# Kernel tuning notes

Hardware: AMD Instinct MI355X
Metric: run time of the kernel (lower is better)

Reference implementation:

```python
import jax, jax.numpy as jnp
import numpy as np

N, C, H, W = 16, 512, 32, 32
NH = 8            # num_heads
HD = C // NH      # head dim c = 64
G = C // 4        # GroupNorm groups = 128
EPS = 1e-5


def conv1x1(X, Wt, b):
    # 1x1 Conv2d == per-pixel linear over channels
    return jnp.einsum('oc,nchw->nohw', Wt, X) + b[None, :, None, None]


def setup_inputs() -> dict:
    key = jax.random.key(0)
    ks = jax.random.split(key, 9)
    s = 0.02
    inp = {
        'X': jax.random.normal(ks[0], (N, C, H, W), jnp.float32),
        'Wq': jax.random.normal(ks[1], (C, C), jnp.float32) * s,
        'bq': jax.random.normal(ks[2], (C,), jnp.float32) * s,
        'Wk': jax.random.normal(ks[3], (C, C), jnp.float32) * s,
        'bk': jax.random.normal(ks[4], (C,), jnp.float32) * s,
        'Wv': jax.random.normal(ks[5], (C, C), jnp.float32) * s,
        'bv': jax.random.normal(ks[6], (C,), jnp.float32) * s,
        'Wo': jax.random.normal(ks[7], (C, C), jnp.float32) * s,
        'bo': jax.random.normal(ks[8], (C,), jnp.float32) * s,
        'gn_w': jnp.ones((C,), jnp.float32),
        'gn_b': jnp.zeros((C,), jnp.float32),
    }
    return inp


def reference(X, Wq, bq, Wk, bk, Wv, bv, Wo, bo, gn_w, gn_b):
    # NOTE: original torch code does  K, Q, V = (Q_conv(X), K_conv(X), V_conv(X))
    # i.e. K gets the Q_conv weights and Q gets the K_conv weights; mirror that.
    K = conv1x1(X, Wq, bq)
    Q = conv1x1(X, Wk, bk)
    V = conv1x1(X, Wv, bv)

    d = H * W
    Kh = K.reshape(N, NH, HD, d)  # [n,h,c,d]
    Qh = Q.reshape(N, NH, HD, d)
    Vh = V.reshape(N, NH, HD, d)

    # softmax-free channel attention: (Q^T K) then V (Q^T K)^T
    A = jnp.einsum('nhcd,nhcD->nhdD', Qh, Kh)   # [n,h,d,d]
    O = jnp.einsum('nhdD,nhcD->nhcd', A, Vh)    # [n,h,c,d]

    O = O.reshape(N, C, H, W)
    O = conv1x1(O, Wo, bo)

    # GroupNorm(G, C) with affine, eps=1e-5
    Og = O.reshape(N, G, C // G, H, W)
    mu = Og.mean(axis=(2, 3, 4), keepdims=True)
    var = Og.var(axis=(2, 3, 4), keepdims=True)
    On = ((Og - mu) * jax.lax.rsqrt(var + EPS)).reshape(N, C, H, W)
    On = On * gn_w[None, :, None, None] + gn_b[None, :, None, None]

    return On + X
```

## Files before the change

### kernel.cpp

```cpp
#include <hip/hip_runtime.h>
#include <hip/hip_bf16.h>

typedef __attribute__((ext_vector_type(8))) short s8v;
typedef __attribute__((ext_vector_type(4))) short s4v;
typedef __attribute__((ext_vector_type(4))) float f32x4;

#define MFMA_BF16 __builtin_amdgcn_mfma_f32_16x16x32_bf16

__device__ inline void gload_lds16(const __hip_bfloat16* g, __hip_bfloat16* l) {
  __builtin_amdgcn_global_load_lds(
      (const __attribute__((address_space(1))) void*)g,
      (__attribute__((address_space(3))) void*)l, 16, 0, 0);
}

__device__ inline short f2bs(float x) {
  __hip_bfloat16 b = __float2bfloat16(x);
  return *reinterpret_cast<short*>(&b);
}

__device__ inline void storeC(float* p, float v) { *p = v; }
__device__ inline void storeC(__hip_bfloat16* p, float v) { *p = __float2bfloat16(v); }

__global__ __launch_bounds__(256) void prep(const float* __restrict__ X,
                                            __hip_bfloat16* __restrict__ XT,
                                            __hip_bfloat16* __restrict__ Xc,
                                            const float* __restrict__ Wq,
                                            const float* __restrict__ Wv,
                                            const float* __restrict__ Wk,
                                            const float* __restrict__ Wo,
                                            const float* __restrict__ bq,
                                            const float* __restrict__ bv,
                                            __hip_bfloat16* __restrict__ WA,
                                            __hip_bfloat16* __restrict__ WkT,
                                            __hip_bfloat16* __restrict__ WOb,
                                            float* __restrict__ biasKV) {
  const int tid = threadIdx.x;
  if (blockIdx.z == 16) {
    const int blk = blockIdx.y * 16 + blockIdx.x;
#pragma unroll
    for (int t = 0; t < 8; ++t) {
      const int i = (blk * 8 + t) * 256 + tid;
      WA[i] = __float2bfloat16(Wq[i]);
      WA[262144 + i] = __float2bfloat16(Wv[i]);
      WOb[i] = __float2bfloat16(Wo[i]);
      WkT[i] = __float2bfloat16(Wk[(i & 511) * 512 + (i >> 9)]);
      if (i < 512) { biasKV[i] = bq[i]; biasKV[512 + i] = bv[i]; }
    }
    return;
  }
  __shared__ float tl[64][65];
  const int n = blockIdx.z;
  const int c0 = blockIdx.y * 64, p0 = blockIdx.x * 64;
  const int lr = tid >> 4, lc4 = (tid & 15) * 4;
  const float* Xp = X + ((long)n * 512 + c0) * 1024 + p0;
  __hip_bfloat16* Xcp = Xc + ((long)n * 512 + c0) * 1024 + p0;
#pragma unroll
  for (int i = 0; i < 4; ++i) {
    const int ch = i * 16 + lr;
    const float4 v = *(const float4*)&Xp[(long)ch * 1024 + lc4];
    tl[ch][lc4 + 0] = v.x; tl[ch][lc4 + 1] = v.y;
    tl[ch][lc4 + 2] = v.z; tl[ch][lc4 + 3] = v.w;
    s4v xo;
    xo[0] = f2bs(v.x); xo[1] = f2bs(v.y); xo[2] = f2bs(v.z); xo[3] = f2bs(v.w);
    *(s4v*)&Xcp[(long)ch * 1024 + lc4] = xo;
  }
  __syncthreads();
  __hip_bfloat16* XTp = XT + ((long)n * 1024 + p0) * 512 + c0;
#pragma unroll
  for (int i = 0; i < 4; ++i) {
    const int px = i * 16 + lr;
    s4v o;
#pragma unroll
    for (int e = 0; e < 4; ++e) o[e] = f2bs(tl[lc4 + e][px]);
    *(s4v*)&XTp[(long)px * 512 + lc4] = o;
  }
}

template <typename OutT, bool BROW>
__global__ __launch_bounds__(256) void gemm_nt(
    const __hip_bfloat16* __restrict__ A, long strideA,
    const __hip_bfloat16* __restrict__ B, long strideB,
    OutT* __restrict__ C, long strideC, int K, int ldc,
    const float* __restrict__ brow, long strideBrow) {
  A += blockIdx.z * strideA;
  B += blockIdx.z * strideB;
  C += blockIdx.z * strideC;
  const int m0 = blockIdx.y * 128;
  const int n0 = blockIdx.x * 128;
  const int tid = threadIdx.x;
  const int wid = tid >> 6, lane = tid & 63;
  const int wm = wid >> 1, wn = wid & 1;

  __shared__ __hip_bfloat16 As[128 * 64];
  __shared__ __hip_bfloat16 Bs[128 * 64];

  f32x4 acc[4][4] = {};

  const __hip_bfloat16* gA0 = A + (long)(m0 + wid * 32 + (lane >> 3)) * K + (lane & 7) * 8;
  const __hip_bfloat16* gB0 = B + (long)(n0 + wid * 32 + (lane >> 3)) * K + (lane & 7) * 8;

  for (int k0 = 0; k0 < K; k0 += 64) {
#pragma unroll
    for (int t = 0; t < 4; ++t) {
      gload_lds16(gA0 + (long)t * 8 * K + k0, &As[(wid * 32 + t * 8) * 64]);
      gload_lds16(gB0 + (long)t * 8 * K + k0, &Bs[(wid * 32 + t * 8) * 64]);
    }
    __syncthreads();
#pragma unroll
    for (int ks = 0; ks < 2; ++ks) {
      const int koff = ks * 32 + (lane >> 4) * 8;
      s8v a[4], b[4];
#pragma unroll
      for (int i = 0; i < 4; ++i)
        a[i] = *(const s8v*)&As[(wm * 64 + i * 16 + (lane & 15)) * 64 + koff];
#pragma unroll
      for (int j = 0; j < 4; ++j)
        b[j] = *(const s8v*)&Bs[(wn * 64 + j * 16 + (lane & 15)) * 64 + koff];
#pragma unroll
      for (int i = 0; i < 4; ++i)
#pragma unroll
        for (int j = 0; j < 4; ++j)
          acc[i][j] = MFMA_BF16(a[i], b[j], acc[i][j], 0, 0, 0);
    }
    __syncthreads();
  }

  const int cr = (lane >> 4) * 4;
  const int cc = lane & 15;
#pragma unroll
  for (int i = 0; i < 4; ++i) {
#pragma unroll
    for (int r = 0; r < 4; ++r) {
      const int gm = m0 + wm * 64 + i * 16 + cr + r;
      const float rb = BROW ? brow[blockIdx.z * strideBrow + gm] : 0.f;
#pragma unroll
      for (int j = 0; j < 4; ++j) {
        const int gn = n0 + wn * 64 + j * 16 + cc;
        storeC(&C[(long)gm * ldc + gn], acc[i][j][r] + rb);
      }
    }
  }
}

__global__ __launch_bounds__(512) void gemm_vkT(const __hip_bfloat16* __restrict__ V,
                                                const __hip_bfloat16* __restrict__ Kk,
                                                __hip_bfloat16* __restrict__ Mt) {
  const int n = blockIdx.x >> 3, h = blockIdx.x & 7;
  const int tid = threadIdx.x, wid = tid >> 6, lane = tid & 63;
  f32x4 acc[4][4] = {};
  const long colbase = (long)n * 1024 + wid * 128 + (lane >> 4) * 8;
  const __hip_bfloat16* Vb = V + (long)(h * 64 + (lane & 15)) * 16384 + colbase;
  const __hip_bfloat16* Kb = Kk + (long)(h * 64 + (lane & 15)) * 16384 + colbase;
#pragma unroll
  for (int kk = 0; kk < 128; kk += 32) {
    s8v a[4], b[4];
#pragma unroll
    for (int i = 0; i < 4; ++i) a[i] = *(const s8v*)(Vb + (long)i * 16 * 16384 + kk);
#pragma unroll
    for (int j = 0; j < 4; ++j) b[j] = *(const s8v*)(Kb + (long)j * 16 * 16384 + kk);
#pragma unroll
    for (int i = 0; i < 4; ++i)
#pragma unroll
      for (int j = 0; j < 4; ++j) acc[i][j] = MFMA_BF16(a[i], b[j], acc[i][j], 0, 0, 0);
  }
  __shared__ float part[4][4096];
  const int cr = (lane >> 4) * 4, cc = lane & 15;
  if (wid < 4) {
#pragma unroll
    for (int i = 0; i < 4; ++i)
#pragma unroll
      for (int r = 0; r < 4; ++r)
#pragma unroll
        for (int j = 0; j < 4; ++j)
          part[wid][(i * 16 + cr + r) * 64 + j * 16 + cc] = acc[i][j][r];
  }
  __syncthreads();
  if (wid >= 4) {
#pragma unroll
    for (int i = 0; i < 4; ++i)
#pragma unroll
      for (int r = 0; r < 4; ++r)
#pragma unroll
        for (int j = 0; j < 4; ++j)
          part[wid - 4][(i * 16 + cr + r) * 64 + j * 16 + cc] += acc[i][j][r];
  }
  __syncthreads();
  __hip_bfloat16* outp = Mt + ((long)n * 8 + h) * 4096;
  for (int e = tid; e < 4096; e += 512) {
    const float sum = part[0][e] + part[1][e] + part[2][e] + part[3][e];
    outp[(e & 63) * 64 + (e >> 6)] = __float2bfloat16(sum);
  }
}

__global__ __launch_bounds__(256) void wchain(const __hip_bfloat16* __restrict__ WOb,
                                              const __hip_bfloat16* __restrict__ WkT,
                                              const __hip_bfloat16* __restrict__ Mt,
                                              const float* __restrict__ bk,
                                              const float* __restrict__ bo,
                                              __hip_bfloat16* __restrict__ WPP,
                                              float* __restrict__ b2out) {
  const int c0 = blockIdx.x * 128, o0 = blockIdx.y * 128, n = blockIdx.z;
  const int tid = threadIdx.x, wid = tid >> 6, lane = tid & 63;
  const int wm = wid >> 1, wn = wid & 1;
  const int cr = (lane >> 4) * 4, cc = lane & 15;

  __shared__ __hip_bfloat16 WoS[128 * 64];
  __shared__ __hip_bfloat16 WkS[128 * 64];
  __shared__ __hip_bfloat16 MtS[64 * 64];
  __shared__ __hip_bfloat16 W1S[128 * 64];
  __shared__ float bkS[512];

  if (tid < 128) *(float4*)&bkS[tid * 4] = *(const float4*)&bk[tid * 4];

  f32x4 acc2[4][4] = {};
  float bacc = 0.f;
  const int r8 = lane >> 3, b8 = (lane & 7) * 8;

  for (int h = 0; h < 8; ++h) {
#pragma unroll
    for (int t = 0; t < 4; ++t) {
      const int row = wid * 32 + t * 8;
      gload_lds16(WOb + (long)(o0 + row + r8) * 512 + h * 64 + b8, &WoS[row * 64]);
      gload_lds16(WkT + (long)(c0 + row + r8) * 512 + h * 64 + b8, &WkS[row * 64]);
    }
    {
      const __hip_bfloat16* mg = Mt + ((long)n * 8 + h) * 4096;
      gload_lds16(mg + wid * 512 + lane * 8, &MtS[wid * 512]);
      gload_lds16(mg + 2048 + wid * 512 + lane * 8, &MtS[2048 + wid * 512]);
    }
    __syncthreads();

    f32x4 acc1[2][4] = {};
#pragma unroll
    for (int ks = 0; ks < 2; ++ks) {
      const int ko = ks * 32 + (lane >> 4) * 8;
      s8v aj[2], bw[4];
#pragma unroll
      for (int i = 0; i < 2; ++i)
        aj[i] = *(const s8v*)&MtS[(wn * 32 + i * 16 + cc) * 64 + ko];
#pragma unroll
      for (int t = 0; t < 4; ++t)
        bw[t] = *(const s8v*)&WoS[(wm * 64 + t * 16 + cc) * 64 + ko];
#pragma unroll
      for (int i = 0; i < 2; ++i)
#pragma unroll
        for (int t = 0; t < 4; ++t)
          acc1[i][t] = MFMA_BF16(aj[i], bw[t], acc1[i][t], 0, 0, 0);
    }
#pragma unroll
    for (int i = 0; i < 2; ++i)
#pragma unroll
      for (int t = 0; t < 4; ++t) {
        const int o = wm * 64 + t * 16 + cc;
        const int jb = wn * 32 + i * 16 + cr;
        s4v p;
#pragma unroll
        for (int r = 0; r < 4; ++r) p[r] = f2bs(acc1[i][t][r]);
        *(s4v*)((char*)W1S + ((o * 128 + jb * 2) ^ ((o & 7) << 4))) = p;
      }
    __syncthreads();

#pragma unroll
    for (int ks = 0; ks < 2; ++ks) {
      const int ko = ks * 32 + (lane >> 4) * 8;
      s8v a2[4], bw[4];
#pragma unroll
      for (int i = 0; i < 4; ++i) {
        const int o = wm * 64 + i * 16 + cc;
        a2[i] = *(const s8v*)((char*)W1S + ((o * 128 + ko * 2) ^ ((o & 7) << 4)));
      }
#pragma unroll
      for (int t = 0; t < 4; ++t)
        bw[t] = *(const s8v*)&WkS[(wn * 64 + t * 16 + cc) * 64 + ko];
#pragma unroll
      for (int i = 0; i < 4; ++i)
#pragma unroll
        for (int t = 0; t < 4; ++t)
          acc2[i][t] = MFMA_BF16(a2[i], bw[t], acc2[i][t], 0, 0, 0);
    }

    if (c0 == 0) {
      const int o = tid >> 1, half = tid & 1;
      float s = 0.f;
#pragma unroll
      for (int q = 0; q < 4; ++q) {
        const int jb = half * 64 + q * 16;
        const s8v w = *(const s8v*)((char*)W1S + ((o * 128 + jb) ^ ((o & 7) << 4)));
        const __hip_bfloat16* wb = (const __hip_bfloat16*)&w;
#pragma unroll
        for (int e = 0; e < 8; ++e)
          s += __bfloat162float(wb[e]) * bkS[h * 64 + half * 32 + q * 8 + e];
      }
      bacc += s;
    }
    __syncthreads();
  }

#pragma unroll
  for (int i = 0; i < 4; ++i)
#pragma unroll
    for (int r = 0; r < 4; ++r)
#pragma unroll
      for (int t = 0; t < 4; ++t)
        WPP[((long)n * 512 + o0 + wm * 64 + i * 16 + cr + r) * 512 +
            c0 + wn * 64 + t * 16 + cc] = __float2bfloat16(acc2[i][t][r]);
  if (c0 == 0) {
    const float tot = bacc + __shfl_xor(bacc, 1);
    if ((tid & 1) == 0) {
      const int o = tid >> 1;
      b2out[n * 512 + o0 + o] = tot + bo[o0 + o];
    }
  }
}

__global__ __launch_bounds__(512, 4) void ygn(const __hip_bfloat16* __restrict__ WPP,
                                              const __hip_bfloat16* __restrict__ XT,
                                              const float* __restrict__ b2,
                                              const __hip_bfloat16* __restrict__ Xc,
                                              const float* __restrict__ gw,
                                              const float* __restrict__ gb,
                                              float* __restrict__ out) {
  const int ch0 = blockIdx.x * 32, n = blockIdx.y;
  const int tid = threadIdx.x, wid = tid >> 6, lane = tid & 63;
  const int wm = wid & 1, wpx = wid >> 1;
  const int cc = lane & 15, cr = (lane >> 4) * 4;

  __shared__ __hip_bfloat16 As[32 * 512];
  __shared__ __hip_bfloat16 Bs[256 * 64];
  __shared__ float chS[32][2];
  __shared__ float gS[8][2];

  const __hip_bfloat16* wp = WPP + ((long)n * 512 + ch0) * 512;
#pragma unroll
  for (int t = 0; t < 4; ++t) {
    const int row = wid * 4 + t;
    gload_lds16(wp + (long)row * 512 + lane * 8, &As[row * 512]);
  }
  if (tid < 64) chS[tid >> 1][tid & 1] = 0.f;

  const __hip_bfloat16* xb = XT + (long)n * 1024 * 512;
  f32x4 acc[4][4] = {};

#pragma unroll
  for (int pc = 0; pc < 4; ++pc) {
    for (int kc = 0; kc < 8; ++kc) {
#pragma unroll
      for (int t = 0; t < 4; ++t) {
        const int r0 = wid * 32 + t * 8;
        gload_lds16(xb + (long)(pc * 256 + r0 + (lane >> 3)) * 512 + kc * 64 + (lane & 7) * 8,
                    &Bs[r0 * 64]);
      }
      __syncthreads();
#pragma unroll
      for (int ks = 0; ks < 2; ++ks) {
        const int ko = ks * 32 + (lane >> 4) * 8;
        const s8v a = *(const s8v*)&As[(wm * 16 + cc) * 512 + kc * 64 + ko];
#pragma unroll
        for (int j = 0; j < 4; ++j) {
          const s8v b = *(const s8v*)&Bs[(wpx * 64 + j * 16 + cc) * 64 + ko];
          acc[pc][j] = MFMA_BF16(a, b, acc[pc][j], 0, 0, 0);
        }
      }
      __syncthreads();
    }
  }

  float b2v[4], gwv[4], gbv[4];
#pragma unroll
  for (int r = 0; r < 4; ++r) {
    const int ch = ch0 + wm * 16 + cr + r;
    b2v[r] = b2[n * 512 + ch];
    gwv[r] = gw[ch];
    gbv[r] = gb[ch];
  }
  float s[4] = {}, s2[4] = {};
#pragma unroll
  for (int pc = 0; pc < 4; ++pc)
#pragma unroll
    for (int j = 0; j < 4; ++j)
#pragma unroll
      for (int r = 0; r < 4; ++r) {
        const float v = acc[pc][j][r] + b2v[r];
        acc[pc][j][r] = v;
        s[r] += v;
        s2[r] += v * v;
      }
#pragma unroll
  for (int off = 1; off < 16; off <<= 1)
#pragma unroll
    for (int r = 0; r < 4; ++r) {
      s[r] += __shfl_xor(s[r], off);
      s2[r] += __shfl_xor(s2[r], off);
    }
  if (cc == 0) {
#pragma unroll
    for (int r = 0; r < 4; ++r) {
      atomicAdd(&chS[wm * 16 + cr + r][0], s[r]);
      atomicAdd(&chS[wm * 16 + cr + r][1], s2[r]);
    }
  }
  __syncthreads();
  if (tid < 8) {
    const int g = tid;
    float ts = 0.f, t2 = 0.f;
#pragma unroll
    for (int c = 0; c < 4; ++c) { ts += chS[g * 4 + c][0]; t2 += chS[g * 4 + c][1]; }
    const float mu = ts * (1.f / 4096.f);
    const float var = t2 * (1.f / 4096.f) - mu * mu;
    gS[g][0] = mu;
    gS[g][1] = rsqrtf(var + 1e-5f);
  }
  __syncthreads();

#pragma unroll
  for (int r = 0; r < 4; ++r) {
    const int chl = wm * 16 + cr + r;
    const int ch = ch0 + chl;
    const float mu = gS[chl >> 2][0], rstd = gS[chl >> 2][1];
    const float sc = rstd * gwv[r], sh = gbv[r];
    float* op = out + ((long)n * 512 + ch) * 1024;
    const __hip_bfloat16* xr = Xc + ((long)n * 512 + ch) * 1024;
#pragma unroll
    for (int pc = 0; pc < 4; ++pc)
#pragma unroll
      for (int j = 0; j < 4; ++j) {
        const int px = pc * 256 + wpx * 64 + j * 16 + cc;
        op[px] = (acc[pc][j][r] - mu) * sc + sh + __bfloat162float(xr[px]);
      }
  }
}

extern "C" void kernel_launch(void* const* d_in, const int* in_sizes, int n_in,
                              void* d_out, int out_size, void* d_ws, size_t ws_size,
                              hipStream_t stream) {
  const float* X  = (const float*)d_in[0];
  const float* Wq = (const float*)d_in[1];
  const float* bq = (const float*)d_in[2];
  const float* Wk = (const float*)d_in[3];
  const float* bk = (const float*)d_in[4];
  const float* Wv = (const float*)d_in[5];
  const float* bv = (const float*)d_in[6];
  const float* Wo = (const float*)d_in[7];
  const float* bo = (const float*)d_in[8];
  const float* gw = (const float*)d_in[9];
  const float* gb = (const float*)d_in[10];
  float* out = (float*)d_out;

  char* ws = (char*)d_ws;
  __hip_bfloat16* XT  = (__hip_bfloat16*)(ws + 0);
  __hip_bfloat16* KV  = (__hip_bfloat16*)(ws + 16777216);
  __hip_bfloat16* WPP = (__hip_bfloat16*)(ws + 58720256);
  __hip_bfloat16* Mt  = (__hip_bfloat16*)(ws + 67108864);
  __hip_bfloat16* WA  = (__hip_bfloat16*)(ws + 68157440);
  __hip_bfloat16* WkT = (__hip_bfloat16*)(ws + 69206016);
  __hip_bfloat16* WOb = (__hip_bfloat16*)(ws + 69730304);
  float*          bKV = (float*)(ws + 70254592);
  float*          b2  = (float*)(ws + 70258688);
  __hip_bfloat16* Xc  = (__hip_bfloat16*)(ws + 75497472);

  prep<<<dim3(16, 8, 17), 256, 0, stream>>>(X, XT, Xc, Wq, Wv, Wk, Wo, bq, bv,
                                            WA, WkT, WOb, bKV);
  gemm_nt<__hip_bfloat16, true><<<dim3(128, 8, 1), 256, 0, stream>>>(
      WA, 0, XT, 0, KV, 0, 512, 16384, bKV, 0);
  gemm_vkT<<<128, 512, 0, stream>>>(KV + (long)512 * 16384, KV, Mt);
  wchain<<<dim3(4, 4, 16), 256, 0, stream>>>(WOb, WkT, Mt, bk, bo, WPP, b2);
  ygn<<<dim3(16, 16), 512, 0, stream>>>(WPP, XT, b2, Xc, gw, gb, out);
}
```

Measured before the change: 137.7 us.

## Double-buffer ygn X tiles with XOR swizzle, padded A, XCD-aware block mapping

In the final GEMM+GroupNorm kernel, the X tile loads into LDS are now double-buffered, so the next k-chunk is fetched while MFMAs run on the current one. This replaces two barriers per iteration with one. The B tile is stored with an XOR swizzle and the A tile row is padded to 520 to reduce LDS bank conflicts. Blocks are remapped from a 2D grid to a 1D id so that each batch's blocks land on the same XCD for L2 locality. The cost is double the B LDS footprint and the dropped min-blocks launch bound, which may lower occupancy.

```diff
diff --git a/kernel.cpp b/kernel.cpp
--- a/kernel.cpp
+++ b/kernel.cpp
@@ -313,55 +313,73 @@
   }
 }
 
-__global__ __launch_bounds__(512, 4) void ygn(const __hip_bfloat16* __restrict__ WPP,
-                                              const __hip_bfloat16* __restrict__ XT,
-                                              const float* __restrict__ b2,
-                                              const __hip_bfloat16* __restrict__ Xc,
-                                              const float* __restrict__ gw,
-                                              const float* __restrict__ gb,
-                                              float* __restrict__ out) {
-  const int ch0 = blockIdx.x * 32, n = blockIdx.y;
+__global__ __launch_bounds__(512) void ygn(const __hip_bfloat16* __restrict__ WPP,
+                                           const __hip_bfloat16* __restrict__ XT,
+                                           const float* __restrict__ b2,
+                                           const __hip_bfloat16* __restrict__ Xc,
+                                           const float* __restrict__ gw,
+                                           const float* __restrict__ gb,
+                                           float* __restrict__ out) {
+  const int id = blockIdx.x;
+  const int xcd = id & 7, slot = id >> 3;
+  const int n = xcd * 2 + (slot >> 4);
+  const int ch0 = (slot & 15) * 32;
   const int tid = threadIdx.x, wid = tid >> 6, lane = tid & 63;
   const int wm = wid & 1, wpx = wid >> 1;
   const int cc = lane & 15, cr = (lane >> 4) * 4;
 
-  __shared__ __hip_bfloat16 As[32 * 512];
-  __shared__ __hip_bfloat16 Bs[256 * 64];
+  __shared__ __hip_bfloat16 As[32 * 520];
+  __shared__ __hip_bfloat16 Bs[2][256 * 64];
   __shared__ float chS[32][2];
   __shared__ float gS[8][2];
 
-  const __hip_bfloat16* wp = WPP + ((long)n * 512 + ch0) * 512;
-#pragma unroll
-  for (int t = 0; t < 4; ++t) {
-    const int row = wid * 4 + t;
-    gload_lds16(wp + (long)row * 512 + lane * 8, &As[row * 512]);
+  {
+    const __hip_bfloat16* wp = WPP + ((long)n * 512 + ch0) * 512;
+    const int row = tid >> 4, e0 = (tid & 15) * 32;
+#pragma unroll
+    for (int q = 0; q < 4; ++q)
+      *(s8v*)&As[row * 520 + e0 + q * 8] =
+          *(const s8v*)(wp + (long)row * 512 + e0 + q * 8);
   }
   if (tid < 64) chS[tid >> 1][tid & 1] = 0.f;
 
   const __hip_bfloat16* xb = XT + (long)n * 1024 * 512;
+  const int swz = ((lane & 7) ^ (lane >> 3)) * 8;
+  auto STAGE = [&](int it, int buf) {
+    const int pcs = it >> 3, kcs = it & 7;
+#pragma unroll
+    for (int t = 0; t < 4; ++t) {
+      const int r0 = wid * 32 + t * 8;
+      gload_lds16(xb + (long)(pcs * 256 + r0 + (lane >> 3)) * 512 + kcs * 64 + swz,
+                  &Bs[buf][r0 * 64]);
+    }
+  };
+
   f32x4 acc[4][4] = {};
+  STAGE(0, 0);
 
 #pragma unroll
   for (int pc = 0; pc < 4; ++pc) {
     for (int kc = 0; kc < 8; ++kc) {
-#pragma unroll
-      for (int t = 0; t < 4; ++t) {
-        const int r0 = wid * 32 + t * 8;
-        gload_lds16(xb + (long)(pc * 256 + r0 + (lane >> 3)) * 512 + kc * 64 + (lane & 7) * 8,
-                    &Bs[r0 * 64]);
-      }
-      __syncthreads();
+      const int it = pc * 8 + kc;
+      const int cur = kc & 1;
+      asm volatile("s_waitcnt vmcnt(0) lgkmcnt(0)" ::: "memory");
+      __builtin_amdgcn_s_barrier();
+      __builtin_amdgcn_sched_barrier(0);
+      if (it < 31) STAGE(it + 1, cur ^ 1);
 #pragma unroll
       for (int ks = 0; ks < 2; ++ks) {
         const int ko = ks * 32 + (lane >> 4) * 8;
-        const s8v a = *(const s8v*)&As[(wm * 16 + cc) * 512 + kc * 64 + ko];
+        const int g = ks * 4 + (lane >> 4);
+        const s8v a = *(const s8v*)&As[(wm * 16 + cc) * 520 + kc * 64 + ko];
 #pragma unroll
         for (int j = 0; j < 4; ++j) {
-          const s8v b = *(const s8v*)&Bs[(wpx * 64 + j * 16 + cc) * 64 + ko];
+          const int row = wpx * 64 + j * 16 + cc;
+          const s8v b = *(const s8v*)((const char*)&Bs[cur][0] +
+                                      ((row << 7) | ((g ^ (cc & 7)) << 4)));
           acc[pc][j] = MFMA_BF16(a, b, acc[pc][j], 0, 0, 0);
         }
       }
-      __syncthreads();
     }
   }
 
@@ -392,6 +410,7 @@
       s[r] += __shfl_xor(s[r], off);
       s2[r] += __shfl_xor(s2[r], off);
     }
+  __syncthreads();
   if (cc == 0) {
 #pragma unroll
     for (int r = 0; r < 4; ++r) {
@@ -464,5 +483,5 @@
       WA, 0, XT, 0, KV, 0, 512, 16384, bKV, 0);
   gemm_vkT<<<128, 512, 0, stream>>>(KV + (long)512 * 16384, KV, Mt);
   wchain<<<dim3(4, 4, 16), 256, 0, stream>>>(WOb, WkT, Mt, bk, bo, WPP, b2);
-  ygn<<<dim3(16, 16), 512, 0, stream>>>(WPP, XT, b2, Xc, gw, gb, out);
-}
+  ygn<<<256, 512, 0, stream>>>(WPP, XT, b2, Xc, gw, gb, out);
+}
```

Result: faster. 118.7 us (-13.7%).
